# Optimization experiments

Measured on AMD Instinct MI355X. Metric: run time of the kernel, lower is better.

## Reference

```python
import jax, jax.numpy as jnp
import numpy as np

NUM_INPUTS = 8
NUM_MFS = 3
NUM_RULES = NUM_MFS ** NUM_INPUTS  # 6561
BATCH = 8192


def setup_inputs() -> dict:
    key = jax.random.key(0)
    k1, k2, k3 = jax.random.split(key, 3)
    x = jax.random.normal(k1, (BATCH, NUM_INPUTS), dtype=jnp.float32)
    # one GaussianMF per input: centers ~ randn(num_mfs)
    centers = jax.random.normal(k2, (NUM_INPUTS, NUM_MFS), dtype=jnp.float32)
    # sigmas fixed buffer [0.3, 0.5, 0.7] shared across all inputs
    sigmas = jnp.array([0.3, 0.5, 0.7], dtype=jnp.float32)
    consequents = jax.random.normal(k3, (NUM_RULES, NUM_INPUTS + 1), dtype=jnp.float32)
    return {"x": x, "centers": centers, "sigmas": sigmas, "consequents": consequents}


def reference(x, centers, sigmas, consequents):
    B, nI = x.shape
    M = centers.shape[1]
    # Gaussian memberships: [B, nI, M]
    mu = jnp.exp(-0.5 * ((x[:, :, None] - centers[None, :, :]) / sigmas[None, None, :]) ** 2)
    # Rule strengths via successive outer products (lexicographic order matches
    # itertools.product(range(M), repeat=nI): first input varies slowest).
    s = mu[:, 0, :]  # [B, M]
    for j in range(1, nI):
        s = (s[:, :, None] * mu[:, j, None, :]).reshape(B, -1)  # [B, M^(j+1)]
    # s: [B, NUM_RULES]
    ones = jnp.ones((B, 1), dtype=x.dtype)
    xb = jnp.concatenate([x, ones], axis=1)  # [B, nI+1]
    rule_outputs = jnp.einsum('bi,ri->br', xb, consequents)  # [B, R]
    out = jnp.sum(s * rule_outputs, axis=1) / (jnp.sum(s, axis=1) + 1e-6)
    return out[:, None]
```

## Files before the change

kernel.cpp:

```cpp
#include <hip/hip_runtime.h>
#include <math.h>
#include <stdint.h>

#define BATCH 8192
#define NI    8
#define NM    3
#define NT    243
#define IL2C  (-0.72134752f)

typedef uint32_t u32;
typedef __fp16 h2    __attribute__((ext_vector_type(2)));
typedef __fp16 f16x8 __attribute__((ext_vector_type(8)));
typedef float  f32x4 __attribute__((ext_vector_type(4)));
typedef u32    u32x4 __attribute__((ext_vector_type(4)));

__device__ __forceinline__ u32 pack2(float a, float b) {
    h2 p = __builtin_amdgcn_cvt_pkrtz(a, b);
    return __builtin_bit_cast(u32, p);
}
__device__ __forceinline__ float sel3(const float* v, int i) {
    return (i == 0) ? v[0] : ((i == 1) ? v[1] : v[2]);
}

__global__ __launch_bounds__(256) void sugeno_prep(
    const float* __restrict__ cons,
    u32* __restrict__ Bpack)
{
    int idx = blockIdx.x * 256 + threadIdx.x;
    if (idx >= NT * 64) return;
    int t  = idx >> 6;
    int l  = idx & 63;
    int n  = l & 15;
    int kb = (l >> 4) * 8;
    u32 w[4];
    #pragma unroll
    for (int p = 0; p < 4; ++p) {
        int k0 = kb + 2 * p, k1 = k0 + 1;
        float f0 = (k0 < 27 && n < 9) ? cons[(size_t)(t * 27 + k0) * 9 + n] : 0.0f;
        float f1 = (k1 < 27 && n < 9) ? cons[(size_t)(t * 27 + k1) * 9 + n] : 0.0f;
        w[p] = pack2(f0, f1);
    }
    u32x4 ww; ww[0] = w[0]; ww[1] = w[1]; ww[2] = w[2]; ww[3] = w[3];
    ((u32x4*)Bpack)[idx] = ww;
}

__global__ __launch_bounds__(256) void sugeno_main(
    const float* __restrict__ x,
    const float* __restrict__ centers,
    const float* __restrict__ sigmas,
    const u32*   __restrict__ Bpack,
    float* __restrict__ out)
{
    __shared__ float Wred[4][256];
    const int tid  = threadIdx.x;
    const int l    = tid & 63;
    const int wv   = tid >> 6;
    const int tile = blockIdx.x;
    const int brow = tile * 16 + (l & 15);

    const float4* xv = (const float4*)(x + (size_t)brow * NI);
    float4 x0 = xv[0], x1 = xv[1];
    float xr[NI] = {x0.x, x0.y, x0.z, x0.w, x1.x, x1.y, x1.z, x1.w};

    float il2[NM];
    #pragma unroll
    for (int m = 0; m < NM; ++m) {
        float s = sigmas[m];
        il2[m] = IL2C / (s * s);
    }

    float mA[NI][NM];
    #pragma unroll
    for (int j = 0; j < NI; ++j) {
        float a0, a1, a2;
        {
            float d0 = xr[j] - centers[j * NM + 0];
            float d1 = xr[j] - centers[j * NM + 1];
            float d2 = xr[j] - centers[j * NM + 2];
            a0 = d0 * d0 * il2[0];
            a1 = d1 * d1 * il2[1];
            a2 = d2 * d2 * il2[2];
        }
        float Kj = fmaxf(fmaxf(a0, a1), a2);
        mA[j][0] = exp2f(a0 - Kj);
        mA[j][1] = exp2f(a1 - Kj);
        mA[j][2] = exp2f(a2 - Kj);
    }

    const int kb = (l >> 4) * 8;
    float L[8];
    #pragma unroll
    for (int j = 0; j < 8; ++j) {
        int k = kb + j;
        if (k < 27)
            L[j] = sel3(mA[5], k / 9) * sel3(mA[6], (k % 9) / 3) * sel3(mA[7], k % 3);
        else
            L[j] = 0.0f;
    }

    const int t0     = wv * 60;
    const int ngroup = (wv == 3) ? 21 : 20;

    int g3 = t0 / 3;
    int d3 = g3 % 3, d2 = (g3 / 3) % 3, d1 = (g3 / 9) % 3, d0 = g3 / 27;
    float P3 = sel3(mA[0], d0) * sel3(mA[1], d1) * sel3(mA[2], d2) * sel3(mA[3], d3);

    const u32x4* bp = (const u32x4*)Bpack + (size_t)t0 * 64 + l;

    f32x4 acc = {0.0f, 0.0f, 0.0f, 0.0f};

    for (int g = 0; g < ngroup; ++g) {
        #pragma unroll
        for (int ph = 0; ph < 3; ++ph) {
            float U = P3 * mA[4][ph];
            u32x4 aw;
            aw[0] = pack2(U * L[0], U * L[1]);
            aw[1] = pack2(U * L[2], U * L[3]);
            aw[2] = pack2(U * L[4], U * L[5]);
            aw[3] = pack2(U * L[6], U * L[7]);
            u32x4 bw = bp[(g * 3 + ph) * 64];
            acc = __builtin_amdgcn_mfma_f32_16x16x32_f16(
                      __builtin_bit_cast(f16x8, aw),
                      __builtin_bit_cast(f16x8, bw),
                      acc, 0, 0, 0);
        }
        if (++d3 == 3) { d3 = 0; if (++d2 == 3) { d2 = 0; if (++d1 == 3) { d1 = 0; ++d0; } } }
        P3 = sel3(mA[0], d0) * sel3(mA[1], d1) * sel3(mA[2], d2) * sel3(mA[3], d3);
    }

    {
        const int col = l & 15, rgrp = l >> 4;
        #pragma unroll
        for (int r = 0; r < 4; ++r)
            Wred[wv][(rgrp * 4 + r) * 16 + col] = acc[r];
    }
    __syncthreads();

    const int row = tid >> 4, cc = tid & 15;
    float Wsum = Wred[0][tid] + Wred[1][tid] + Wred[2][tid] + Wred[3][tid];
    const int bb = tile * 16 + row;
    float xbv = (cc < 8) ? x[(size_t)bb * NI + cc] : (cc == 8 ? 1.0f : 0.0f);
    float p = Wsum * xbv;
    p += __shfl_xor(p, 1);
    p += __shfl_xor(p, 2);
    p += __shfl_xor(p, 4);
    p += __shfl_xor(p, 8);

    if (cc == 0) {
        const float4* yv = (const float4*)(x + (size_t)bb * NI);
        float4 y0 = yv[0], y1 = yv[1];
        float yr[NI] = {y0.x, y0.y, y0.z, y0.w, y1.x, y1.y, y1.z, y1.w};
        float S = 1.0f, Ksum = 0.0f;
        #pragma unroll
        for (int j = 0; j < NI; ++j) {
            float e0 = yr[j] - centers[j * NM + 0];
            float e1 = yr[j] - centers[j * NM + 1];
            float e2 = yr[j] - centers[j * NM + 2];
            float a0 = e0 * e0 * il2[0];
            float a1 = e1 * e1 * il2[1];
            float a2 = e2 * e2 * il2[2];
            S *= exp2f(a0) + exp2f(a1) + exp2f(a2);
            Ksum += fmaxf(fmaxf(a0, a1), a2);
        }
        out[bb] = p * exp2f(Ksum) / (S + 1e-6f);
    }
}

extern "C" void kernel_launch(void* const* d_in, const int* in_sizes, int n_in,
                              void* d_out, int out_size, void* d_ws, size_t ws_size,
                              hipStream_t stream)
{
    const float* x       = (const float*)d_in[0];
    const float* centers = (const float*)d_in[1];
    const float* sigmas  = (const float*)d_in[2];
    const float* cons    = (const float*)d_in[3];
    float* out           = (float*)d_out;
    u32*   Bpack         = (u32*)d_ws;

    sugeno_prep<<<(NT * 64 + 255) / 256, 256, 0, stream>>>(cons, Bpack);

    sugeno_main<<<BATCH / 16, 256, 0, stream>>>(x, centers, sigmas, Bpack, out);
}
```

Baseline: 29.31 us.

## Split rule tiles across eight waves, prefetch B fragments, pack A in fp16

Doubles the block to 512 threads so eight waves each handle about 30 rule tiles instead of 60, which raises wave-level parallelism per batch tile. It also software-prefetches the next group's three B fragments from global memory, and precomputes the L factors as packed fp16 so each A operand is built with packed half multiplies. The costs are extra LDS for the reduction, eight-way partial sums, fp16 rounding of products applied in a different order, and more register pressure from the prefetch buffers.

```diff
diff --git a/kernel.cpp b/kernel.cpp
--- a/kernel.cpp
+++ b/kernel.cpp
@@ -44,14 +44,14 @@
     ((u32x4*)Bpack)[idx] = ww;
 }
 
-__global__ __launch_bounds__(256) void sugeno_main(
+__global__ __launch_bounds__(512, 4) void sugeno_main(
     const float* __restrict__ x,
     const float* __restrict__ centers,
     const float* __restrict__ sigmas,
     const u32*   __restrict__ Bpack,
     float* __restrict__ out)
 {
-    __shared__ float Wred[4][256];
+    __shared__ float Wred[8][256];
     const int tid  = threadIdx.x;
     const int l    = tid & 63;
     const int wv   = tid >> 6;
@@ -72,15 +72,12 @@
     float mA[NI][NM];
     #pragma unroll
     for (int j = 0; j < NI; ++j) {
-        float a0, a1, a2;
-        {
-            float d0 = xr[j] - centers[j * NM + 0];
-            float d1 = xr[j] - centers[j * NM + 1];
-            float d2 = xr[j] - centers[j * NM + 2];
-            a0 = d0 * d0 * il2[0];
-            a1 = d1 * d1 * il2[1];
-            a2 = d2 * d2 * il2[2];
-        }
+        float d0 = xr[j] - centers[j * NM + 0];
+        float d1 = xr[j] - centers[j * NM + 1];
+        float d2 = xr[j] - centers[j * NM + 2];
+        float a0 = d0 * d0 * il2[0];
+        float a1 = d1 * d1 * il2[1];
+        float a2 = d2 * d2 * il2[2];
         float Kj = fmaxf(fmaxf(a0, a1), a2);
         mA[j][0] = exp2f(a0 - Kj);
         mA[j][1] = exp2f(a1 - Kj);
@@ -88,18 +85,22 @@
     }
 
     const int kb = (l >> 4) * 8;
-    float L[8];
+    u32 Lp[4];
     #pragma unroll
-    for (int j = 0; j < 8; ++j) {
-        int k = kb + j;
-        if (k < 27)
-            L[j] = sel3(mA[5], k / 9) * sel3(mA[6], (k % 9) / 3) * sel3(mA[7], k % 3);
-        else
-            L[j] = 0.0f;
+    for (int i = 0; i < 4; ++i) {
+        float lv[2];
+        #pragma unroll
+        for (int h = 0; h < 2; ++h) {
+            int k = kb + 2 * i + h;
+            lv[h] = (k < 27)
+                  ? sel3(mA[5], k / 9) * sel3(mA[6], (k % 9) / 3) * sel3(mA[7], k % 3)
+                  : 0.0f;
+        }
+        Lp[i] = pack2(lv[0], lv[1]);
     }
 
-    const int t0     = wv * 60;
-    const int ngroup = (wv == 3) ? 21 : 20;
+    const int t0     = wv * 30;
+    const int ngroup = (wv == 7) ? 11 : 10;
 
     int g3 = t0 / 3;
     int d3 = g3 % 3, d2 = (g3 / 3) % 3, d1 = (g3 / 9) % 3, d0 = g3 / 27;
@@ -109,21 +110,31 @@
 
     f32x4 acc = {0.0f, 0.0f, 0.0f, 0.0f};
 
+    u32x4 c0 = bp[0], c1 = bp[64], c2 = bp[128];
     for (int g = 0; g < ngroup; ++g) {
+        u32x4 n0, n1, n2;
+        if (g + 1 < ngroup) {
+            const u32x4* nb = bp + (size_t)(g + 1) * 192;
+            n0 = nb[0]; n1 = nb[64]; n2 = nb[128];
+        }
         #pragma unroll
         for (int ph = 0; ph < 3; ++ph) {
             float U = P3 * mA[4][ph];
+            u32 uu = pack2(U, U);
+            h2 uh = __builtin_bit_cast(h2, uu);
             u32x4 aw;
-            aw[0] = pack2(U * L[0], U * L[1]);
-            aw[1] = pack2(U * L[2], U * L[3]);
-            aw[2] = pack2(U * L[4], U * L[5]);
-            aw[3] = pack2(U * L[6], U * L[7]);
-            u32x4 bw = bp[(g * 3 + ph) * 64];
+            #pragma unroll
+            for (int i = 0; i < 4; ++i) {
+                h2 prod = __builtin_bit_cast(h2, Lp[i]) * uh;
+                aw[i] = __builtin_bit_cast(u32, prod);
+            }
+            u32x4 bw = (ph == 0) ? c0 : (ph == 1) ? c1 : c2;
             acc = __builtin_amdgcn_mfma_f32_16x16x32_f16(
                       __builtin_bit_cast(f16x8, aw),
                       __builtin_bit_cast(f16x8, bw),
                       acc, 0, 0, 0);
         }
+        c0 = n0; c1 = n1; c2 = n2;
         if (++d3 == 3) { d3 = 0; if (++d2 == 3) { d2 = 0; if (++d1 == 3) { d1 = 0; ++d0; } } }
         P3 = sel3(mA[0], d0) * sel3(mA[1], d1) * sel3(mA[2], d2) * sel3(mA[3], d3);
     }
@@ -136,33 +147,38 @@
     }
     __syncthreads();
 
-    const int row = tid >> 4, cc = tid & 15;
-    float Wsum = Wred[0][tid] + Wred[1][tid] + Wred[2][tid] + Wred[3][tid];
-    const int bb = tile * 16 + row;
-    float xbv = (cc < 8) ? x[(size_t)bb * NI + cc] : (cc == 8 ? 1.0f : 0.0f);
-    float p = Wsum * xbv;
-    p += __shfl_xor(p, 1);
-    p += __shfl_xor(p, 2);
-    p += __shfl_xor(p, 4);
-    p += __shfl_xor(p, 8);
+    if (tid < 256) {
+        const int row = tid >> 4, cc = tid & 15;
+        float Wsum = 0.0f;
+        #pragma unroll
+        for (int w = 0; w < 8; ++w) Wsum += Wred[w][tid];
 
-    if (cc == 0) {
-        const float4* yv = (const float4*)(x + (size_t)bb * NI);
-        float4 y0 = yv[0], y1 = yv[1];
-        float yr[NI] = {y0.x, y0.y, y0.z, y0.w, y1.x, y1.y, y1.z, y1.w};
-        float S = 1.0f, Ksum = 0.0f;
-        #pragma unroll
-        for (int j = 0; j < NI; ++j) {
-            float e0 = yr[j] - centers[j * NM + 0];
-            float e1 = yr[j] - centers[j * NM + 1];
-            float e2 = yr[j] - centers[j * NM + 2];
-            float a0 = e0 * e0 * il2[0];
-            float a1 = e1 * e1 * il2[1];
-            float a2 = e2 * e2 * il2[2];
-            S *= exp2f(a0) + exp2f(a1) + exp2f(a2);
-            Ksum += fmaxf(fmaxf(a0, a1), a2);
+        const int bb = tile * 16 + row;
+        float xbv = (cc < 8) ? x[(size_t)bb * NI + cc] : (cc == 8 ? 1.0f : 0.0f);
+        float p = Wsum * xbv;
+        p += __shfl_xor(p, 1);
+        p += __shfl_xor(p, 2);
+        p += __shfl_xor(p, 4);
+        p += __shfl_xor(p, 8);
+
+        if (cc == 0) {
+            const float4* yv = (const float4*)(x + (size_t)bb * NI);
+            float4 y0 = yv[0], y1 = yv[1];
+            float yr[NI] = {y0.x, y0.y, y0.z, y0.w, y1.x, y1.y, y1.z, y1.w};
+            float S = 1.0f, Ksum = 0.0f;
+            #pragma unroll
+            for (int j = 0; j < NI; ++j) {
+                float e0 = yr[j] - centers[j * NM + 0];
+                float e1 = yr[j] - centers[j * NM + 1];
+                float e2 = yr[j] - centers[j * NM + 2];
+                float a0 = e0 * e0 * il2[0];
+                float a1 = e1 * e1 * il2[1];
+                float a2 = e2 * e2 * il2[2];
+                S *= exp2f(a0) + exp2f(a1) + exp2f(a2);
+                Ksum += fmaxf(fmaxf(a0, a1), a2);
+            }
+            out[bb] = p * exp2f(Ksum) / (S + 1e-6f);
         }
-        out[bb] = p * exp2f(Ksum) / (S + 1e-6f);
     }
 }
 
@@ -179,5 +195,5 @@
 
     sugeno_prep<<<(NT * 64 + 255) / 256, 256, 0, stream>>>(cons, Bpack);
 
-    sugeno_main<<<BATCH / 16, 256, 0, stream>>>(x, centers, sigmas, Bpack, out);
+    sugeno_main<<<BATCH / 16, 512, 0, stream>>>(x, centers, sigmas, Bpack, out);
 }
```

Result: faster. 26.04 us (-11.2%).
